# Optimization experiments

Hardware: AMD Instinct MI355X
Metric: run time of the kernel (lower is better)

## Reference

```python
import jax, jax.numpy as jnp
import numpy as np
from jax.scipy.special import gammaln

BLOCK = 96          # NIQE block size at scale 1 (48 at scale 2)
KSIZE = 7           # gaussian MSCN window size
SIGMA = 7.0 / 6.0   # gaussian sigma
PAD = KSIZE // 2
NUM_FEAT = 18       # features per block per scale

# gamma grid for AGGD shape-parameter search (matches torch.arange(0.2, 10.001, 0.001))
AGGD_GRID = jnp.asarray(np.arange(0.2, 10.0 + 0.001, 0.001), dtype=jnp.float32)
R_GAM = jnp.exp(2.0 * gammaln(2.0 / AGGD_GRID) - (gammaln(1.0 / AGGD_GRID) + gammaln(3.0 / AGGD_GRID)))


def _gauss_kernel():
    m = (KSIZE - 1) / 2.0
    y, x = np.ogrid[-m:m + 1, -m:m + 1]
    h = np.exp(-(x * x + y * y) / (2.0 * SIGMA * SIGMA))
    h[h < np.finfo(h.dtype).eps * h.max()] = 0
    h = h / h.sum()
    return jnp.asarray(h, dtype=jnp.float32)[None, None]  # (1,1,7,7)

GAUSS = _gauss_kernel()


def imfilter(x):
    # replicate ('same') padding + valid conv, like _image_filter
    xp = jnp.pad(x, ((0, 0), (0, 0), (PAD, PAD), (PAD, PAD)), mode='edge')
    return jax.lax.conv_general_dilated(xp, GAUSS, (1, 1), 'VALID')


def estimate_aggd(blocks):
    # blocks: (N, k, k)
    mask_l = blocks < 0
    mask_r = blocks > 0
    cl = jnp.sum(mask_l, axis=(-1, -2)).astype(blocks.dtype)
    cr = jnp.sum(mask_r, axis=(-1, -2)).astype(blocks.dtype)
    left_std = jnp.sqrt(jnp.sum(jnp.where(mask_l, blocks, 0.0) ** 2, axis=(-1, -2)) / (cl + 1e-8))
    right_std = jnp.sqrt(jnp.sum(jnp.where(mask_r, blocks, 0.0) ** 2, axis=(-1, -2)) / (cr + 1e-8))
    gamma_hat = left_std / right_std
    rhat = jnp.mean(jnp.abs(blocks), axis=(-1, -2)) ** 2 / jnp.mean(blocks ** 2, axis=(-1, -2))
    rhat_norm = rhat * (gamma_hat ** 3 + 1.0) * (gamma_hat + 1.0) / (gamma_hat ** 2 + 1.0) ** 2
    pos = jnp.argmin(jnp.abs(R_GAM[None, :] - rhat_norm[:, None]), axis=-1)  # (N, 9801) search
    alpha = AGGD_GRID[pos]
    conv = jnp.sqrt(jnp.exp(gammaln(1.0 / alpha) - gammaln(3.0 / alpha)))
    return alpha, left_std * conv, right_std * conv


def mscn_features(blocks):
    # blocks: (N, k, k) -> (N, 18)
    alpha, lb, rb = estimate_aggd(blocks)
    feats = [alpha, (lb + rb) / 2.0]
    for sh in ((0, 1), (1, 0), (1, 1), (1, -1)):
        shifted = jnp.roll(blocks, sh, axis=(-2, -1))
        a, l, r = estimate_aggd(blocks * shifted)
        mean = (r - l) * jnp.exp(gammaln(2.0 / a) - gammaln(1.0 / a))
        feats.extend((a, mean, l, r))
    return jnp.stack(feats, axis=-1)


def blockify(img, bs):
    # img: (b,1,H,W) -> (b, nb, bs, bs); partial blocks discarded like _blockproc_torch
    b, _, h, w = img.shape
    nbh, nbw = h // bs, w // bs
    x = img[:, 0, :nbh * bs, :nbw * bs].reshape(b, nbh, bs, nbw, bs)
    return x.transpose(0, 1, 3, 2, 4).reshape(b, nbh * nbw, bs, bs)


def mscn_normalize(img):
    mu = imfilter(img)
    sigma = jnp.sqrt(jnp.abs(imfilter(img * img) - mu * mu))
    return (img - mu) / (sigma + 1.0)


def niqe_score(image, mu_pris, cov_pris):
    img = image
    feats = []
    for scale in (1, 2):
        norm = mscn_normalize(img)
        blocks = blockify(norm, BLOCK // scale)
        b, nb, k, _ = blocks.shape
        f = mscn_features(blocks.reshape(b * nb, k, k)).reshape(b, nb, NUM_FEAT)
        feats.append(f)
        if scale == 1:
            # 2x2 average-pool downsample for second scale
            bb, cc, hh, ww = img.shape
            img = img.reshape(bb, cc, hh // 2, 2, ww // 2, 2).mean(axis=(3, 5))
    feats = jnp.concatenate(feats, axis=-1)  # (b, nb, 36)
    nb = feats.shape[1]
    mu_dist = feats.mean(axis=1)                        # (b, 36)
    xm = feats - mu_dist[:, None, :]
    cov_dist = jnp.einsum('bnf,bng->bfg', xm, xm) / (nb - 1)
    cov = (cov_pris[None] + cov_dist) / 2.0
    diff = mu_pris[None, :] - mu_dist                   # (b, 36)
    invc = jnp.linalg.pinv(cov)
    quad = jnp.einsum('bf,bfg,bg->b', diff, invc, diff)
    return jnp.sqrt(jnp.maximum(quad, 0.0))


def setup_inputs() -> dict:
    key = jax.random.key(0)
    k1, k2, k3 = jax.random.split(key, 3)
    image = jax.random.uniform(k1, (16, 1, 1056, 1056), dtype=jnp.float32)
    mu_pris = jax.random.normal(k2, (36,), dtype=jnp.float32)
    a = jax.random.normal(k3, (36, 36), dtype=jnp.float32)
    cov_pris = a @ a.T / 36.0 + 0.5 * jnp.eye(36, dtype=jnp.float32)  # SPD pristine covariance
    return {'image': image, 'mu_pris': mu_pris, 'cov_pris': cov_pris}


def reference(image, mu_pris, cov_pris):
    return niqe_score(image, mu_pris, cov_pris)
```

## Files before the change

kernel.cpp:

```cpp
#include <hip/hip_runtime.h>
#include <math.h>

#define NGRID 9801
#define NB 11
#define NBLK (NB*NB)
#define BATCH 16
#define NFEAT 36

__global__ void init_tables(float* __restrict__ rgam, float* __restrict__ convt,
                            float* __restrict__ meanf, float* __restrict__ w1d) {
    int i = blockIdx.x * blockDim.x + threadIdx.x;
    if (i < NGRID) {
        double a = (double)(float)(0.2 + 0.001 * (double)i);
        double g1 = lgamma(1.0 / a);
        double g2 = lgamma(2.0 / a);
        double g3 = lgamma(3.0 / a);
        rgam[i]  = (float)exp(2.0 * g2 - g1 - g3);
        convt[i] = (float)sqrt(exp(g1 - g3));
        meanf[i] = (float)exp(g2 - g1);
    }
    if (i == 0) {
        double g[7], s = 0.0;
        for (int k = 0; k < 7; ++k) { double d = (double)(k - 3); g[k] = exp(-d * d * 18.0 / 49.0); s += g[k]; }
        for (int k = 0; k < 7; ++k) w1d[k] = (float)(g[k] / s);
    }
}

__device__ __forceinline__ float bperm(int addr, float v) {
    return __int_as_float(__builtin_amdgcn_ds_bpermute(addr, __float_as_int(v)));
}

template <int K, bool WDS>
__global__ __launch_bounds__(256) void fused_mscn_stats(
        const float* __restrict__ img, float* __restrict__ dsout,
        const float* __restrict__ w1d, float* __restrict__ stats,
        int H, int W) {
    constexpr int NSLAB = K / 48;
    constexpr int NSTRIP = 4 / NSLAB;
    constexpr int SROWS = K / NSTRIP;
    __shared__ float blk[K][K];
    __shared__ float red[4][25];

    const int tid = threadIdx.x;
    const int lane = tid & 63;
    const int wv = tid >> 6;
    const int slab = wv % NSLAB;
    const int strip = wv / NSLAB;
    const int bIdx = blockIdx.x;
    const int b = blockIdx.y;
    const int bh = bIdx / NB, bw = bIdx % NB;
    const int x0 = bw * K + slab * 48;
    const int gx = x0 - 3 + lane;
    const int gxc = min(max(gx, 0), W - 1);
    const int r0 = bh * K + strip * SROWS;
    const int basem3 = (lane - 3) << 2;

    const float* im = img + (size_t)b * H * W + gxc;
    const float w0=w1d[0], w1=w1d[1], w2=w1d[2], w3=w1d[3], w4=w1d[4], w5=w1d[5], w6=w1d[6];

    auto ld = [&](int r) -> float {
        int rc = min(max(r, 0), H - 1);
        return im[(size_t)rc * W];
    };
    auto hconv = [&](float v, float& omu, float& om2) {
        float a0 = bperm(basem3,      v);
        float a1 = bperm(basem3 + 4,  v);
        float a2 = bperm(basem3 + 8,  v);
        float a4 = bperm(basem3 + 16, v);
        float a5 = bperm(basem3 + 20, v);
        float a6 = bperm(basem3 + 24, v);
        omu = ((w0*a0 + w1*a1) + (w2*a2 + w3*v)) + ((w4*a4 + w5*a5) + w6*a6);
        om2 = ((w0*a0*a0 + w1*a1*a1) + (w2*a2*a2 + w3*v*v)) + ((w4*a4*a4 + w5*a5*a5) + w6*a6*a6);
    };

    float m0,m1,mm2,m3,m4,m5,m6, q0,q1,q2,q3,q4,q5,q6;
    float rA, rB, rC, dsSave = 0.f;
    float vN = ld(r0 - 3);
    { float v = vN; vN = ld(r0 - 2); hconv(v, m0,  q0); }
    { float v = vN; vN = ld(r0 - 1); hconv(v, m1,  q1); }
    { float v = vN; vN = ld(r0 + 0); hconv(v, mm2, q2); }
    { float v = vN; vN = ld(r0 + 1); hconv(v, m3,  q3); rA = v; }
    { float v = vN; vN = ld(r0 + 2); hconv(v, m4,  q4); rB = v; }
    { float v = vN; vN = ld(r0 + 3); hconv(v, m5,  q5); rC = v; }

    const bool doout = (lane >= 3) && (lane <= 50);
    const bool dsw = WDS && (lane & 1) && (lane >= 3) && (lane <= 49);

    for (int y = r0; y < r0 + SROWS; ++y) {
        float v = vN; vN = ld(y + 4);
        hconv(v, m6, q6);
        float rD = v;
        float mu = ((w0*m0 + w1*m1) + (w2*mm2 + w3*m3)) + ((w4*m4 + w5*m5) + w6*m6);
        float s2 = ((w0*q0 + w1*q1) + (w2*q2 + w3*q3)) + ((w4*q4 + w5*q5) + w6*q6);
        float sig = __builtin_amdgcn_sqrtf(fabsf(s2 - mu * mu));
        if (doout) blk[y - bh * K][slab * 48 + lane - 3] = (rA - mu) * __builtin_amdgcn_rcpf(sig + 1.0f);
        if constexpr (WDS) {
            float hs = rA + __shfl_down(rA, 1);
            if ((y & 1) == 0) dsSave = hs;
            else if (dsw)
                dsout[((size_t)b * (H / 2) + (y >> 1)) * (W / 2) + (gx >> 1)] = 0.25f * (dsSave + hs);
        }
        m0=m1; m1=mm2; mm2=m3; m3=m4; m4=m5; m5=m6;
        q0=q1; q1=q2; q2=q3; q3=q4; q4=q5; q5=q6;
        rA=rB; rB=rC; rC=rD;
    }
    __syncthreads();

    float acc[5][5];
    #pragma unroll
    for (int s = 0; s < 5; ++s)
        #pragma unroll
        for (int q = 0; q < 5; ++q) acc[s][q] = 0.f;

    for (int idx = tid; idx < K * K; idx += 256) {
        int i = idx / K, j = idx % K;
        int im1 = i ? i - 1 : K - 1;
        int jm1 = j ? j - 1 : K - 1;
        int jp1 = (j == K - 1) ? 0 : j + 1;
        float v0 = blk[i][j];
        float vs[5];
        vs[0] = v0;
        vs[1] = v0 * blk[i][jm1];
        vs[2] = v0 * blk[im1][j];
        vs[3] = v0 * blk[im1][jm1];
        vs[4] = v0 * blk[im1][jp1];
        #pragma unroll
        for (int s = 0; s < 5; ++s) {
            float v = vs[s];
            float v2 = v * v;
            if (v < 0.f)      { acc[s][0] += 1.f; acc[s][2] += v2; }
            else if (v > 0.f) { acc[s][1] += 1.f; acc[s][3] += v2; }
            acc[s][4] += fabsf(v);
        }
    }
    #pragma unroll
    for (int off = 32; off >= 1; off >>= 1)
        #pragma unroll
        for (int s = 0; s < 5; ++s)
            #pragma unroll
            for (int q = 0; q < 5; ++q)
                acc[s][q] += __shfl_down(acc[s][q], off);

    if (lane == 0) {
        #pragma unroll
        for (int s = 0; s < 5; ++s)
            #pragma unroll
            for (int q = 0; q < 5; ++q) red[wv][s * 5 + q] = acc[s][q];
    }
    __syncthreads();
    if (tid < 25) {
        stats[((size_t)b * NBLK + bIdx) * 25 + tid] =
            red[0][tid] + red[1][tid] + red[2][tid] + red[3][tid];
    }
}

__global__ __launch_bounds__(256) void aggd_kernel(
        const float* __restrict__ stats1, const float* __restrict__ stats2,
        const float* __restrict__ rgam, const float* __restrict__ convt,
        const float* __restrict__ meanf, float* __restrict__ feats) {
    __shared__ float rg[NGRID];
    for (int i = threadIdx.x; i < NGRID; i += 256) rg[i] = rgam[i];
    __syncthreads();

    int gid = blockIdx.x * 256 + threadIdx.x;
    if (gid >= 2 * BATCH * NBLK * 5) return;
    int s = gid % 5; int t = gid / 5;
    int blk = t % NBLK; t /= NBLK;
    int b = t % BATCH; int scale = t / BATCH;

    const float* st = (scale ? stats2 : stats1) + ((size_t)b * NBLK + blk) * 25 + s * 5;
    float cl = st[0], cr = st[1], sl2 = st[2], sr2 = st[3], sab = st[4];
    float n = scale ? (48.f * 48.f) : (96.f * 96.f);

    float lstd = sqrtf(sl2 / (cl + 1e-8f));
    float rstd = sqrtf(sr2 / (cr + 1e-8f));
    float gh = lstd / rstd;
    float mab = sab / n;
    float msq = (sl2 + sr2) / n;
    float rhat = mab * mab / msq;
    float g2 = gh * gh;
    float x = rhat * (gh * g2 + 1.f) * (gh + 1.f) / ((g2 + 1.f) * (g2 + 1.f));

    int lo = 0, hi = NGRID;
    while (lo < hi) {
        int mid = (lo + hi) >> 1;
        if (rg[mid] < x) lo = mid + 1; else hi = mid;
    }
    int gi;
    if (lo <= 0) gi = 0;
    else if (lo >= NGRID) gi = NGRID - 1;
    else {
        float dlo = x - rg[lo - 1];
        float dhi = rg[lo] - x;
        gi = (dlo <= dhi) ? lo - 1 : lo;
    }

    float alpha = (float)(0.2 + 0.001 * (double)gi);
    float cv = convt[gi];
    float lb = lstd * cv, rb = rstd * cv;
    float* fo = feats + ((size_t)b * NBLK + blk) * NFEAT + (scale ? 18 : 0);
    if (s == 0) {
        fo[0] = alpha;
        fo[1] = 0.5f * (lb + rb);
    } else {
        int o = 2 + (s - 1) * 4;
        fo[o]     = alpha;
        fo[o + 1] = (rb - lb) * meanf[gi];
        fo[o + 2] = lb;
        fo[o + 3] = rb;
    }
}

__global__ __launch_bounds__(256) void score_kernel(
        const float* __restrict__ feats, const float* __restrict__ mu_pris,
        const float* __restrict__ cov_pris, float* __restrict__ out) {
    __shared__ float F[NBLK][NFEAT];
    __shared__ double mu[NFEAT];
    __shared__ double A[NFEAT][NFEAT + 1];
    __shared__ double dff[NFEAT];
    __shared__ double fac[NFEAT];
    __shared__ double xs[NFEAT];
    int b = blockIdx.x, tid = threadIdx.x;
    const float* fp = feats + (size_t)b * NBLK * NFEAT;
    for (int i = tid; i < NBLK * NFEAT; i += 256) F[i / NFEAT][i % NFEAT] = fp[i];
    __syncthreads();
    if (tid < NFEAT) {
        double s = 0.0;
        for (int n = 0; n < NBLK; ++n) s += (double)F[n][tid];
        mu[tid] = s / (double)NBLK;
        dff[tid] = (double)mu_pris[tid] - mu[tid];
    }
    __syncthreads();
    for (int e = tid; e < NFEAT * NFEAT; e += 256) {
        int f = e / NFEAT, g = e % NFEAT;
        double mf = mu[f], mg = mu[g];
        double s = 0.0;
        for (int n = 0; n < NBLK; ++n) s += ((double)F[n][f] - mf) * ((double)F[n][g] - mg);
        A[f][g] = (s / (double)(NBLK - 1) + (double)cov_pris[f * NFEAT + g]) * 0.5;
    }
    if (tid < NFEAT) A[tid][NFEAT] = dff[tid];
    __syncthreads();
    for (int k = 0; k < NFEAT - 1; ++k) {
        if (tid > k && tid < NFEAT) fac[tid] = A[tid][k] / A[k][k];
        __syncthreads();
        for (int e = tid; e < NFEAT * (NFEAT + 1); e += 256) {
            int r = e / (NFEAT + 1), c = e % (NFEAT + 1);
            if (r > k && c > k) A[r][c] -= fac[r] * A[k][c];
        }
        __syncthreads();
    }
    for (int i = NFEAT - 1; i >= 0; --i) {
        if (tid == i) xs[i] = A[i][NFEAT] / A[i][i];
        __syncthreads();
        if (tid < i) A[tid][NFEAT] -= A[tid][i] * xs[i];
        __syncthreads();
    }
    if (tid == 0) {
        double quad = 0.0;
        for (int i = 0; i < NFEAT; ++i) quad += dff[i] * xs[i];
        out[b] = (float)sqrt(fmax(quad, 0.0));
    }
}

extern "C" void kernel_launch(void* const* d_in, const int* in_sizes, int n_in,
                              void* d_out, int out_size, void* d_ws, size_t ws_size,
                              hipStream_t stream) {
    const float* img      = (const float*)d_in[0];
    const float* mu_pris  = (const float*)d_in[1];
    const float* cov_pris = (const float*)d_in[2];
    float* out = (float*)d_out;
    float* ws = (float*)d_ws;

    const int H1 = 1056, W1 = 1056, H2 = 528, W2 = 528;
    float* rgam  = ws;
    float* convt = rgam + 9856;
    float* meanf = convt + 9856;
    float* w1d   = meanf + 9856;
    float* stats1 = w1d + 8;
    float* stats2 = stats1 + BATCH * NBLK * 25;
    float* feats  = stats2 + BATCH * NBLK * 25;
    float* dsimg  = feats + BATCH * NBLK * NFEAT;

    init_tables<<<(NGRID + 255) / 256, 256, 0, stream>>>(rgam, convt, meanf, w1d);

    fused_mscn_stats<96, true><<<dim3(NBLK, BATCH), 256, 0, stream>>>(
        img, dsimg, w1d, stats1, H1, W1);
    fused_mscn_stats<48, false><<<dim3(NBLK, BATCH), 256, 0, stream>>>(
        dsimg, nullptr, w1d, stats2, H2, W2);

    aggd_kernel<<<(2 * BATCH * NBLK * 5 + 255) / 256, 256, 0, stream>>>(
        stats1, stats2, rgam, convt, meanf, feats);

    score_kernel<<<BATCH, 256, 0, stream>>>(feats, mu_pris, cov_pris, out);
}
```

Baseline: 191.0 us.

## Accumulate AGGD statistics in registers during MSCN pass instead of shared block

Drops the full KxK shared-memory MSCN tile and the separate second pass over it. Each lane now gathers the five shifted-product statistics on the fly inside the row loop, using cross-lane permutes for horizontal neighbours and carrying the previous row in a register. Strip and slab seams and the wraparound roll neighbours are patched afterwards through small shared edge buffers. Image dimensions become compile-time constants and the update is branchless. This removes shared-memory traffic and a serial phase, but adds permutes and boundary bookkeeping that must exactly reproduce the circular roll semantics.

```diff
diff --git a/kernel.cpp b/kernel.cpp
--- a/kernel.cpp
+++ b/kernel.cpp
@@ -33,12 +33,16 @@
 template <int K, bool WDS>
 __global__ __launch_bounds__(256) void fused_mscn_stats(
         const float* __restrict__ img, float* __restrict__ dsout,
-        const float* __restrict__ w1d, float* __restrict__ stats,
-        int H, int W) {
+        const float* __restrict__ w1d, float* __restrict__ stats) {
     constexpr int NSLAB = K / 48;
     constexpr int NSTRIP = 4 / NSLAB;
     constexpr int SROWS = K / NSTRIP;
-    __shared__ float blk[K][K];
+    constexpr int W = K * NB;
+    constexpr int H = W;
+
+    __shared__ float lastrow[NSTRIP][K];
+    __shared__ float edgeL[NSTRIP][NSLAB][SROWS];
+    __shared__ float edgeR[NSTRIP][NSLAB][SROWS];
     __shared__ float red[4][25];
 
     const int tid = threadIdx.x;
@@ -54,6 +58,15 @@
     const int gxc = min(max(gx, 0), W - 1);
     const int r0 = bh * K + strip * SROWS;
     const int basem3 = (lane - 3) << 2;
+    const bool act = (lane >= 3) && (lane <= 50);
+    int am1, ap1;
+    if constexpr (NSLAB == 1) {
+        am1 = ((lane == 3) ? 50 : (lane - 1)) << 2;
+        ap1 = ((lane == 50) ? 3 : (lane + 1)) << 2;
+    } else {
+        am1 = ((lane - 1) & 63) << 2;
+        ap1 = ((lane + 1) & 63) << 2;
+    }
 
     const float* im = img + (size_t)b * H * W + gxc;
     const float w0=w1d[0], w1=w1d[1], w2=w1d[2], w3=w1d[3], w4=w1d[4], w5=w1d[5], w6=w1d[6];
@@ -73,6 +86,22 @@
         om2 = ((w0*a0*a0 + w1*a1*a1) + (w2*a2*a2 + w3*v*v)) + ((w4*a4*a4 + w5*a5*a5) + w6*a6*a6);
     };
 
+    float acc[5][5];
+    #pragma unroll
+    for (int s = 0; s < 5; ++s)
+        #pragma unroll
+        for (int q = 0; q < 5; ++q) acc[s][q] = 0.f;
+
+    auto upd = [&](int s, float v) {
+        float vn = fminf(v, 0.f);
+        float vp = fmaxf(v, 0.f);
+        acc[s][2] = fmaf(vn, vn, acc[s][2]);
+        acc[s][3] = fmaf(vp, vp, acc[s][3]);
+        acc[s][4] += vp - vn;
+        acc[s][0] += (v < 0.f) ? 1.f : 0.f;
+        acc[s][1] += (v > 0.f) ? 1.f : 0.f;
+    };
+
     float m0,m1,mm2,m3,m4,m5,m6, q0,q1,q2,q3,q4,q5,q6;
     float rA, rB, rC, dsSave = 0.f;
     float vN = ld(r0 - 3);
@@ -83,56 +112,88 @@
     { float v = vN; vN = ld(r0 + 2); hconv(v, m4,  q4); rB = v; }
     { float v = vN; vN = ld(r0 + 3); hconv(v, m5,  q5); rC = v; }
 
-    const bool doout = (lane >= 3) && (lane <= 50);
     const bool dsw = WDS && (lane & 1) && (lane >= 3) && (lane <= 49);
-
-    for (int y = r0; y < r0 + SROWS; ++y) {
+    float prev = 0.f, firstN = 0.f;
+
+    #pragma unroll 6
+    for (int yy = 0; yy < SROWS; ++yy) {
+        const int y = r0 + yy;
         float v = vN; vN = ld(y + 4);
         hconv(v, m6, q6);
         float rD = v;
         float mu = ((w0*m0 + w1*m1) + (w2*mm2 + w3*m3)) + ((w4*m4 + w5*m5) + w6*m6);
         float s2 = ((w0*q0 + w1*q1) + (w2*q2 + w3*q3)) + ((w4*q4 + w5*q5) + w6*q6);
         float sig = __builtin_amdgcn_sqrtf(fabsf(s2 - mu * mu));
-        if (doout) blk[y - bh * K][slab * 48 + lane - 3] = (rA - mu) * __builtin_amdgcn_rcpf(sig + 1.0f);
+        float nrm = (rA - mu) * __builtin_amdgcn_rcpf(sig + 1.0f);
+        float cur = act ? nrm : 0.f;
+
+        float curL = bperm(am1, cur);
+        float prvL = bperm(am1, prev);
+        float prvR = bperm(ap1, prev);
+        upd(0, cur);
+        upd(1, cur * curL);
+        upd(2, cur * prev);
+        upd(3, cur * prvL);
+        upd(4, cur * prvR);
+
+        if (yy == 0) firstN = cur;
+        if constexpr (NSLAB == 2) {
+            if (lane == 3)  edgeL[strip][slab][yy] = cur;
+            if (lane == 50) edgeR[strip][slab][yy] = cur;
+        }
+        if (yy == SROWS - 1 && act) lastrow[strip][slab * 48 + lane - 3] = cur;
+
         if constexpr (WDS) {
             float hs = rA + __shfl_down(rA, 1);
             if ((y & 1) == 0) dsSave = hs;
             else if (dsw)
                 dsout[((size_t)b * (H / 2) + (y >> 1)) * (W / 2) + (gx >> 1)] = 0.25f * (dsSave + hs);
         }
+
+        prev = cur;
         m0=m1; m1=mm2; mm2=m3; m3=m4; m4=m5; m5=m6;
         q0=q1; q1=q2; q2=q3; q3=q4; q4=q5; q5=q6;
         rA=rB; rB=rC; rC=rD;
     }
     __syncthreads();
 
-    float acc[5][5];
-    #pragma unroll
-    for (int s = 0; s < 5; ++s)
-        #pragma unroll
-        for (int q = 0; q < 5; ++q) acc[s][q] = 0.f;
-
-    for (int idx = tid; idx < K * K; idx += 256) {
-        int i = idx / K, j = idx % K;
-        int im1 = i ? i - 1 : K - 1;
-        int jm1 = j ? j - 1 : K - 1;
-        int jp1 = (j == K - 1) ? 0 : j + 1;
-        float v0 = blk[i][j];
-        float vs[5];
-        vs[0] = v0;
-        vs[1] = v0 * blk[i][jm1];
-        vs[2] = v0 * blk[im1][j];
-        vs[3] = v0 * blk[im1][jm1];
-        vs[4] = v0 * blk[im1][jp1];
-        #pragma unroll
-        for (int s = 0; s < 5; ++s) {
-            float v = vs[s];
-            float v2 = v * v;
-            if (v < 0.f)      { acc[s][0] += 1.f; acc[s][2] += v2; }
-            else if (v > 0.f) { acc[s][1] += 1.f; acc[s][3] += v2; }
-            acc[s][4] += fabsf(v);
+    {
+        const int ps = (strip + NSTRIP - 1) % NSTRIP;
+        int j  = slab * 48 + (lane - 3);
+        int js = act ? j : 0;
+        int jm1 = (js + K - 1) % K;
+        int jp1 = (js + 1) % K;
+        float pv  = act ? lastrow[ps][js]  : 0.f;
+        float pvL = act ? lastrow[ps][jm1] : 0.f;
+        float pvR = act ? lastrow[ps][jp1] : 0.f;
+        upd(2, firstN * pv);
+        upd(3, firstN * pvL);
+        upd(4, firstN * pvR);
+    }
+
+    if constexpr (NSLAB == 2) {
+        if (lane < SROWS) {
+            int r = lane;
+            if (slab == 0) {
+                float c0  = edgeL[strip][0][r];
+                float e95 = edgeR[strip][1][r];
+                upd(1, c0 * e95);
+                if (r > 0) {
+                    upd(3, c0 * edgeR[strip][1][r - 1]);
+                    upd(4, edgeR[strip][0][r] * edgeL[strip][1][r - 1]);
+                }
+            } else {
+                float c48 = edgeL[strip][1][r];
+                float e47 = edgeR[strip][0][r];
+                upd(1, c48 * e47);
+                if (r > 0) {
+                    upd(3, c48 * edgeR[strip][0][r - 1]);
+                    upd(4, edgeR[strip][1][r] * edgeL[strip][0][r - 1]);
+                }
+            }
         }
     }
+
     #pragma unroll
     for (int off = 32; off >= 1; off >>= 1)
         #pragma unroll
@@ -271,7 +332,6 @@
     float* out = (float*)d_out;
     float* ws = (float*)d_ws;
 
-    const int H1 = 1056, W1 = 1056, H2 = 528, W2 = 528;
     float* rgam  = ws;
     float* convt = rgam + 9856;
     float* meanf = convt + 9856;
@@ -284,9 +344,9 @@
     init_tables<<<(NGRID + 255) / 256, 256, 0, stream>>>(rgam, convt, meanf, w1d);
 
     fused_mscn_stats<96, true><<<dim3(NBLK, BATCH), 256, 0, stream>>>(
-        img, dsimg, w1d, stats1, H1, W1);
+        img, dsimg, w1d, stats1);
     fused_mscn_stats<48, false><<<dim3(NBLK, BATCH), 256, 0, stream>>>(
-        dsimg, nullptr, w1d, stats2, H2, W2);
+        dsimg, nullptr, w1d, stats2);
 
     aggd_kernel<<<(2 * BATCH * NBLK * 5 + 255) / 256, 256, 0, stream>>>(
         stats1, stats2, rgam, convt, meanf, feats);
```

New measurement: 209.1 us. 9.4% more time.
